# Optimization experiments

Hardware: AMD Instinct MI355X
Metric: run time of the kernel (lower is better)

Reference implementation:

```python
import jax, jax.numpy as jnp
import numpy as np
from jax import lax

POOL_SIZES = (1, 3, 5, 7, 14)  # PyramidSample bins -> 1+9+25+49+196 = 280 positions


def _pool_mat(in_size, out_size):
    # exact torch adaptive_avg_pool1d bin boundaries as a [out, in] averaging matrix
    P = np.zeros((out_size, in_size), np.float32)
    for i in range(out_size):
        s = (i * in_size) // out_size
        e = -((-(i + 1) * in_size) // out_size)
        P[i, s:e] = 1.0 / (e - s)
    return jnp.asarray(P)


def _psp(x):
    # x: [B, C, H, W] -> [B, C, 280]
    B, C, H, W = x.shape
    outs = []
    for s in POOL_SIZES:
        Ph, Pw = _pool_mat(H, s), _pool_mat(W, s)
        y = jnp.einsum('oh,bchw,pw->bcop', Ph, x, Pw)  # adaptive avg pool to [s,s]
        outs.append(y.reshape(B, C, s * s))
    return jnp.concatenate(outs, axis=-1)


def setup_inputs() -> dict:
    key = jax.random.key(0)
    ks = jax.random.split(key, 7)
    B, C, H, W = 8, 256, 96, 96
    c8 = max(4, C // 8)  # 32
    return {
        'x_1': jax.random.normal(ks[0], (B, C, H, W), jnp.float32),
        'x':   jax.random.normal(ks[1], (B, C, H, W), jnp.float32),
        'wq':  jax.random.normal(ks[2], (C, C), jnp.float32) * 0.05,
        'bq':  jax.random.normal(ks[3], (C,), jnp.float32) * 0.05,
        'wk':  jax.random.normal(ks[4], (c8, C), jnp.float32) * 0.05,
        'bk':  jax.random.normal(ks[5], (c8,), jnp.float32) * 0.05,
        'con': jax.random.normal(ks[6], (c8, C, 3, 3), jnp.float32),
    }


def reference(x_1, x, wq, bq, wk, bk, con):
    B, C, H, W = x.shape
    c8 = wk.shape[0]
    # 1x1 convs
    q = jnp.einsum('oc,bchw->bohw', wq, x_1) + bq[None, :, None, None]
    k = jnp.einsum('oc,bchw->bohw', wk, x) + bk[None, :, None, None]
    proj_query = _psp(q)                         # [B, C, 280]
    proj_key = _psp(k)                           # [B, c8, 280]
    aff = jax.nn.sigmoid(jnp.einsum('bcp,bkp->bck', proj_query, proj_key))  # [B, C, c8]
    # synthesize per-sample dynamic 3x3 weights: [B*C, C, 3, 3]
    agg_w = (aff.reshape(B * C, c8) @ con.reshape(c8, C * 9)).reshape(B * C, C, 3, 3)
    # grouped conv, groups = B
    xg = x_1.reshape(1, B * C, H, W)
    out = lax.conv_general_dilated(
        xg, agg_w, window_strides=(1, 1), padding=((1, 1), (1, 1)),
        dimension_numbers=('NCHW', 'OIHW', 'NCHW'), feature_group_count=B)
    return out.reshape(B, C, H, W)
```

## Files before the change

### kernel.cpp

```cpp
#include <hip/hip_runtime.h>
#include <hip/hip_bf16.h>


#define B 8
#define C 256
#define C8 32
#define H 96
#define W 96
#define HW 9216
#define NPOS 280
#define NP 288
#define NWBIN 30
#define RPS 108
#define OTS 68
#define XCH 260
#define PJS 304

typedef __attribute__((ext_vector_type(8))) short short8;
typedef __attribute__((ext_vector_type(4))) float float4v;
typedef __attribute__((ext_vector_type(4))) unsigned short ushort4v;

static __device__ __forceinline__ unsigned short f2bf(float f) {
    unsigned u = __float_as_uint(f);
    unsigned r = (u + 0x7FFF + ((u >> 16) & 1)) >> 16;
    return (unsigned short)r;
}
static __device__ __forceinline__ float bf2f(unsigned short h) {
    unsigned u = ((unsigned)h) << 16;
    return __uint_as_float(u);
}

template<int H0>
static __device__ __forceinline__ void accum_half_col(const float* __restrict__ col0,
                                                      float acc[NWBIN]) {
    const int SC[5]   = {1, 3, 5, 7, 14};
    const int WOFF[5] = {0, 1, 4, 9, 16};
    #pragma unroll
    for (int k = 0; k < NWBIN; ++k) acc[k] = 0.f;
    #pragma unroll
    for (int g = 0; g < 4; ++g) {
        float v[12];
        #pragma unroll
        for (int q = 0; q < 12; ++q) v[q] = col0[(size_t)(H0 + g * 12 + q) * 96];
        #pragma unroll
        for (int q = 0; q < 12; ++q) {
            const int h = H0 + g * 12 + q;
            #pragma unroll
            for (int si = 0; si < 5; ++si) {
                #pragma unroll
                for (int j = 0; j < SC[si]; ++j) {
                    const int st = (j * 96) / SC[si];
                    const int en = (96 * (j + 1) + SC[si] - 1) / SC[si];
                    if (h >= st && h < en) acc[WOFF[si] + j] += v[q];
                }
            }
        }
    }
}

__global__ __launch_bounds__(256) void pool_kernel(const float* __restrict__ x1,
                                                   const float* __restrict__ x,
                                                   unsigned short* __restrict__ px1t,
                                                   unsigned short* __restrict__ pxt) {
    __shared__ __align__(16) float colp[NWBIN * RPS];
    const int bi = blockIdx.x;
    const int which = bi >> 11;
    const int bc = bi & 2047;
    const float* __restrict__ src = (which ? x : x1) + (size_t)bc * HW;
    const int b = bc >> 8;
    const int c = bc & 255;
    unsigned short* __restrict__ dstT = (which ? pxt : px1t) + ((size_t)b * NP) * C + c;
    const int tid = threadIdx.x;

    const int SC[5]   = {1, 3, 5, 7, 14};
    const int WOFF[5] = {0, 1, 4, 9, 16};
    const int POFF[5] = {0, 1, 10, 35, 84};

    float acc[NWBIN];
    if (tid < 96) {
        accum_half_col<0>(src + tid, acc);
    } else if (tid >= 128 && tid < 224) {
        accum_half_col<48>(src + (tid - 128), acc);
    }

    if (tid >= 128 && tid < 224) {
        const int w1 = tid - 128;
        #pragma unroll
        for (int si = 0; si < 5; ++si) {
            #pragma unroll
            for (int i = 0; i < SC[si]; ++i)
                colp[(WOFF[si] + i) * RPS + w1] = acc[WOFF[si] + i];
        }
    }
    __syncthreads();
    if (tid < 96) {
        #pragma unroll
        for (int si = 0; si < 5; ++si) {
            #pragma unroll
            for (int i = 0; i < SC[si]; ++i) {
                const int st = (i * 96) / SC[si];
                const int en = (96 * (i + 1) + SC[si] - 1) / SC[si];
                const float inv = 1.0f / (float)(en - st);
                const int bin = WOFF[si] + i;
                colp[bin * RPS + tid] = (acc[bin] + colp[bin * RPS + tid]) * inv;
            }
        }
    }
    __syncthreads();

    if (tid < NWBIN) {
        float run = 0.f;
        #pragma unroll
        for (int cc = 0; cc < 24; ++cc) {
            float4 v = *(const float4*)&colp[tid * RPS + 4 * cc];
            v.x += run; v.y += v.x; v.z += v.y; v.w += v.z;
            run = v.w;
            *(float4*)&colp[tid * RPS + 4 * cc] = v;
        }
    }
    __syncthreads();

    for (int p = tid; p < NPOS; p += 256) {
        int si;
        if (p < 1) si = 0; else if (p < 10) si = 1; else if (p < 35) si = 2;
        else if (p < 84) si = 3; else si = 4;
        int s = SC[si];
        int loc = p - POFF[si];
        int i = loc / s;
        int j = loc - i * s;
        int st = (j * 96) / s;
        int en = (96 * (j + 1) + s - 1) / s;
        int binrow = WOFF[si] + i;
        float hi = colp[binrow * RPS + (en - 1)];
        float lo = (st > 0) ? colp[binrow * RPS + (st - 1)] : 0.f;
        dstT[(size_t)p * C] = f2bf((hi - lo) * (1.0f / (float)(en - st)));
    }
    if (tid < NP - NPOS) dstT[(size_t)(NPOS + tid) * C] = 0;
}

__global__ __launch_bounds__(256) void proj_mfma(const unsigned short* __restrict__ px1t,
                                                 const unsigned short* __restrict__ pxt,
                                                 const float* __restrict__ wq,
                                                 const float* __restrict__ bq,
                                                 const float* __restrict__ wk,
                                                 const float* __restrict__ bk,
                                                 unsigned short* __restrict__ PQb,
                                                 unsigned short* __restrict__ PKb) {
    __shared__ __align__(16) unsigned short lds[16 * PJS];
    const int bi = blockIdx.x;
    const int b = bi / 18;
    const int mt = bi % 18;
    const int tid = threadIdx.x;
    const int wid = tid >> 6;
    const int lane = tid & 63;
    const int n = lane & 15, quad = lane >> 4;
    const bool isQ = (mt < 16);
    const int row0 = isQ ? mt * 16 : (mt - 16) * 16;
    const float* __restrict__ wm = isQ ? wq : wk;
    const float* __restrict__ bias = isQ ? bq : bk;
    const unsigned short* __restrict__ src = (isQ ? px1t : pxt) + (size_t)b * NP * C;

    short8 af[8];
    #pragma unroll
    for (int ks = 0; ks < 8; ++ks) {
        const float* wr = &wm[(row0 + n) * C + ks * 32 + quad * 8];
        short8 a;
        #pragma unroll
        for (int j = 0; j < 8; ++j) a[j] = (short)f2bf(wr[j]);
        af[ks] = a;
    }

    float4v acc[5];
    #pragma unroll
    for (int t = 0; t < 5; ++t) acc[t] = (float4v){0.f, 0.f, 0.f, 0.f};

    #pragma unroll
    for (int t = 0; t < 5; ++t) {
        const int nt = t * 4 + wid;
        if (nt < 18) {
            #pragma unroll
            for (int ks = 0; ks < 8; ++ks) {
                short8 bf = *(const short8*)&src[(size_t)(nt * 16 + n) * C + ks * 32 + quad * 8];
                acc[t] = __builtin_amdgcn_mfma_f32_16x16x32_bf16(af[ks], bf, acc[t], 0, 0, 0);
            }
        }
    }

    #pragma unroll
    for (int t = 0; t < 5; ++t) {
        const int nt = t * 4 + wid;
        if (nt < 18) {
            #pragma unroll
            for (int reg = 0; reg < 4; ++reg) {
                float v = acc[t][reg] + bias[row0 + quad * 4 + reg];
                lds[(quad * 4 + reg) * PJS + nt * 16 + n] = f2bf(v);
            }
        }
    }
    __syncthreads();
    unsigned short* __restrict__ dstb = isQ ? PQb + ((size_t)b * C + row0) * NP
                                            : PKb + ((size_t)b * C8 + row0) * NP;
    for (int idx = tid; idx < 16 * 144; idx += 256) {
        int r = idx / 144;
        int c2 = idx - r * 144;
        unsigned int v = 0u;
        if (c2 < 140) v = *(const unsigned int*)&lds[r * PJS + c2 * 2];
        ((unsigned int*)&dstb[(size_t)r * NP])[c2] = v;
    }
}

__global__ __launch_bounds__(256) void aff_mfma(const unsigned short* __restrict__ PQb,
                                                const unsigned short* __restrict__ PKb,
                                                unsigned short* __restrict__ affb) {
    const int bi = blockIdx.x;
    const int b = bi >> 2;
    const int og = bi & 3;
    const int tid = threadIdx.x;
    const int wid = tid >> 6;
    const int lane = tid & 63;
    const int n = lane & 15, quad = lane >> 4;
    const int o = og * 64 + wid * 16 + n;

    float4v acc[2];
    acc[0] = (float4v){0.f, 0.f, 0.f, 0.f};
    acc[1] = (float4v){0.f, 0.f, 0.f, 0.f};

    #pragma unroll
    for (int ks = 0; ks < 9; ++ks) {
        short8 bfr = *(const short8*)&PQb[((size_t)b * C + o) * NP + ks * 32 + quad * 8];
        #pragma unroll
        for (int mt = 0; mt < 2; ++mt) {
            short8 a = *(const short8*)&PKb[((size_t)b * C8 + mt * 16 + n) * NP + ks * 32 + quad * 8];
            acc[mt] = __builtin_amdgcn_mfma_f32_16x16x32_bf16(a, bfr, acc[mt], 0, 0, 0);
        }
    }

    #pragma unroll
    for (int mt = 0; mt < 2; ++mt) {
        ushort4v v;
        #pragma unroll
        for (int reg = 0; reg < 4; ++reg) {
            float s = 1.0f / (1.0f + __expf(-acc[mt][reg]));
            v[reg] = f2bf(s);
        }
        *(ushort4v*)&affb[((size_t)b * C + o) * C8 + mt * 16 + quad * 4] = v;
    }
}

__global__ __launch_bounds__(256) void aswz_kernel(const float* __restrict__ con,
                                                   unsigned short* __restrict__ aswz) {
    int idx = blockIdx.x * 256 + threadIdx.x;
    if (idx >= 73728) return;
    int j = idx & 7;
    int lane = (idx >> 3) & 63;
    int mt = (idx >> 9) & 1;
    int s = idx >> 10;
    int pos = s >> 3;
    int cg = s & 7;
    int m = lane & 15, quad = lane >> 4;
    int ko = mt * 16 + m;
    int c = cg * 32 + quad * 8 + j;
    int dy = pos / 3, dx = pos - dy * 3;
    float v = con[((ko * C + c) * 3 + dy) * 3 + dx];
    aswz[idx] = f2bf(v);
}

__global__ __launch_bounds__(256) void x2bf_kernel(const float* __restrict__ x1,
                                                   unsigned short* __restrict__ xbf) {
    __shared__ __align__(16) unsigned short tl[64 * XCH];
    const int bi = blockIdx.x;
    const int b = bi / 144;
    const int pt = bi % 144;
    const int p0 = pt * 64;
    const int wid = threadIdx.x >> 6;
    const int lane = threadIdx.x & 63;

    #pragma unroll 8
    for (int it = 0; it < 64; ++it) {
        int ch = it * 4 + wid;
        float v = x1[((size_t)(b * C + ch)) * HW + p0 + lane];
        tl[lane * XCH + ch] = f2bf(v);
    }
    __syncthreads();
    #pragma unroll
    for (int it = 0; it < 16; ++it) {
        int pr = it * 4 + wid;
        ushort4v v = *(const ushort4v*)&tl[pr * XCH + lane * 4];
        *(ushort4v*)&xbf[((size_t)b * HW + p0 + pr) * 256 + lane * 4] = v;
    }
}

__global__ __launch_bounds__(256) void yconv_mfma(const unsigned short* __restrict__ xbf,
                                                  const unsigned short* __restrict__ aswz,
                                                  unsigned short* __restrict__ Yp) {
    __shared__ unsigned short xsl[10 * 50 * 40];
    const int bi = blockIdx.x;
    const int kc = bi & 3;
    const int rest = bi >> 2;
    const int tilex = rest & 1;
    const int tiley = (rest >> 1) % 12;
    const int b = rest / 24;
    const int tid = threadIdx.x;
    const int wid = tid >> 6;
    const int lane = tid & 63;
    const int n = lane & 15, quad = lane >> 4;

    float4v acc[2][6];
    #pragma unroll
    for (int mt = 0; mt < 2; ++mt)
        #pragma unroll
        for (int t = 0; t < 6; ++t)
            acc[mt][t] = (float4v){0.f, 0.f, 0.f, 0.f};

    int baseb[6];
    #pragma unroll
    for (int t = 0; t < 6; ++t) {
        int tt = wid * 6 + t;
        int rt = tt / 3;
        int xb = (tt % 3) * 16;
        baseb[t] = (rt * 50 + xb + n) * 40 + quad * 8;
    }

    for (int ci = 0; ci < 2; ++ci) {
        const int cg = kc * 2 + ci;
        __syncthreads();
        for (int task = tid; task < 2000; task += 256) {
            int pix = task >> 2;
            int cq = task & 3;
            int r = pix / 50;
            int col = pix - r * 50;
            int gy = tiley * 8 + r - 1;
            int gx = tilex * 48 + col - 1;
            uint4 v = make_uint4(0u, 0u, 0u, 0u);
            if ((unsigned)gy < 96u && (unsigned)gx < 96u)
                v = *(const uint4*)&xbf[((size_t)b * HW + gy * 96 + gx) * 256 + cg * 32 + cq * 8];
            *(uint4*)&xsl[(r * 50 + col) * 40 + cq * 8] = v;
        }
        short8 af[9][2];
        #pragma unroll
        for (int pos = 0; pos < 9; ++pos)
            #pragma unroll
            for (int mt = 0; mt < 2; ++mt)
                af[pos][mt] = *(const short8*)&aswz[((((pos * 8 + cg) * 2) + mt) * 64 + lane) * 8];
        __syncthreads();

        #pragma unroll
        for (int pos = 0; pos < 9; ++pos) {
            const int dy = pos / 3, dx = pos - (pos / 3) * 3;
            const int d = (dy * 50 + dx) * 40;
            #pragma unroll
            for (int t = 0; t < 6; ++t) {
                short8 bf = *(const short8*)&xsl[baseb[t] + d];
                acc[0][t] = __builtin_amdgcn_mfma_f32_16x16x32_bf16(af[pos][0], bf, acc[0][t], 0, 0, 0);
                acc[1][t] = __builtin_amdgcn_mfma_f32_16x16x32_bf16(af[pos][1], bf, acc[1][t], 0, 0, 0);
            }
        }
    }

    #pragma unroll
    for (int mt = 0; mt < 2; ++mt) {
        #pragma unroll
        for (int t = 0; t < 6; ++t) {
            int tt = wid * 6 + t;
            int rt = tt / 3;
            int xb = (tt % 3) * 16;
            int gy = tiley * 8 + rt;
            int gx = tilex * 48 + xb + n;
            ushort4v v;
            #pragma unroll
            for (int reg = 0; reg < 4; ++reg) v[reg] = f2bf(acc[mt][t][reg]);
            *(ushort4v*)&Yp[((((size_t)kc * B + b) * HW + gy * 96 + gx)) * C8 + mt * 16 + quad * 4] = v;
        }
    }
}

__global__ __launch_bounds__(256) void mix_kernel(const unsigned short* __restrict__ Yp,
                                                  const unsigned short* __restrict__ affb,
                                                  float* __restrict__ out) {
    __shared__ float ot[128 * OTS];
    const int bi = blockIdx.x;
    const int b = bi / 144;
    const int pg = bi % 144;
    const int wid = threadIdx.x >> 6;
    const int lane = threadIdx.x & 63;
    const int n = lane & 15, quad = lane >> 4;
    const int px0 = pg * 64 + wid * 16;

    short8 y0 = *(const short8*)&Yp[(((size_t)0 * B + b) * HW + px0 + n) * C8 + quad * 8];
    short8 y1 = *(const short8*)&Yp[(((size_t)1 * B + b) * HW + px0 + n) * C8 + quad * 8];
    short8 y2 = *(const short8*)&Yp[(((size_t)2 * B + b) * HW + px0 + n) * C8 + quad * 8];
    short8 y3 = *(const short8*)&Yp[(((size_t)3 * B + b) * HW + px0 + n) * C8 + quad * 8];

    float4v acc[16];
    #pragma unroll
    for (int mt = 0; mt < 16; ++mt) acc[mt] = (float4v){0.f, 0.f, 0.f, 0.f};

    #pragma unroll
    for (int mt = 0; mt < 16; ++mt) {
        const short8 a = *(const short8*)&affb[((size_t)b * C + mt * 16 + n) * C8 + quad * 8];
        acc[mt] = __builtin_amdgcn_mfma_f32_16x16x32_bf16(a, y0, acc[mt], 0, 0, 0);
        acc[mt] = __builtin_amdgcn_mfma_f32_16x16x32_bf16(a, y1, acc[mt], 0, 0, 0);
        acc[mt] = __builtin_amdgcn_mfma_f32_16x16x32_bf16(a, y2, acc[mt], 0, 0, 0);
        acc[mt] = __builtin_amdgcn_mfma_f32_16x16x32_bf16(a, y3, acc[mt], 0, 0, 0);
    }

    #pragma unroll
    for (int half = 0; half < 2; ++half) {
        __syncthreads();
        #pragma unroll
        for (int mt = 0; mt < 8; ++mt) {
            #pragma unroll
            for (int reg = 0; reg < 4; ++reg) {
                ot[(mt * 16 + quad * 4 + reg) * OTS + wid * 16 + n] = acc[half * 8 + mt][reg];
            }
        }
        __syncthreads();
        #pragma unroll
        for (int i = 0; i < 32; ++i) {
            int o = wid * 32 + i;
            out[((size_t)b * C + half * 128 + o) * HW + pg * 64 + lane] = ot[o * OTS + lane];
        }
    }
}

extern "C" void kernel_launch(void* const* d_in, const int* in_sizes, int n_in,
                              void* d_out, int out_size, void* d_ws, size_t ws_size,
                              hipStream_t stream) {
    const float* x1  = (const float*)d_in[0];
    const float* x   = (const float*)d_in[1];
    const float* wq  = (const float*)d_in[2];
    const float* bq  = (const float*)d_in[3];
    const float* wk  = (const float*)d_in[4];
    const float* bk  = (const float*)d_in[5];
    const float* con = (const float*)d_in[6];
    float* out = (float*)d_out;

    float* ws = (float*)d_ws;
    unsigned short* affb = (unsigned short*)ws;
    unsigned short* aswz = (unsigned short*)(ws + 65536);
    unsigned short* px1t = (unsigned short*)(ws + 102400);
    unsigned short* pxt  = (unsigned short*)(ws + 397312);
    unsigned short* PQb  = (unsigned short*)(ws + 692224);
    unsigned short* PKb  = (unsigned short*)(ws + 987136);
    unsigned short* xbf = (unsigned short*)(ws + 102400);
    unsigned short* Yp  = (unsigned short*)(ws + 9539584);

    aswz_kernel<<<288, 256, 0, stream>>>(con, aswz);
    pool_kernel<<<4096, 256, 0, stream>>>(x1, x, px1t, pxt);
    proj_mfma<<<B * 18, 256, 0, stream>>>(px1t, pxt, wq, bq, wk, bk, PQb, PKb);
    aff_mfma<<<B * 4, 256, 0, stream>>>(PQb, PKb, affb);
    x2bf_kernel<<<1152, 256, 0, stream>>>(x1, xbf);
    yconv_mfma<<<768, 256, 0, stream>>>(xbf, aswz, Yp);
    mix_kernel<<<1152, 256, 0, stream>>>(Yp, affb, out);
}
```

Before: 269.6 us.

## Fuse independent pre-processing and affinity/conv kernels into combined launches

Merges the pooling, bf16 transpose of x_1 and weight swizzle kernels into one launch dispatched by block index, and merges the affinity GEMM with the dynamic conv kernel. The workspace layout is changed so xbf no longer aliases the pooled buffers, which lets the transpose run concurrently with pooling. The aim is to remove launch gaps and serialization between independent stages. The cost is that every block of the fused kernel reserves the largest shared-memory footprint, which may lower occupancy for pool blocks.

```diff
diff --git a/kernel.cpp b/kernel.cpp
--- a/kernel.cpp
+++ b/kernel.cpp
@@ -25,10 +25,6 @@
     unsigned r = (u + 0x7FFF + ((u >> 16) & 1)) >> 16;
     return (unsigned short)r;
 }
-static __device__ __forceinline__ float bf2f(unsigned short h) {
-    unsigned u = ((unsigned)h) << 16;
-    return __uint_as_float(u);
-}
 
 template<int H0>
 static __device__ __forceinline__ void accum_half_col(const float* __restrict__ col0,
@@ -58,12 +54,11 @@
     }
 }
 
-__global__ __launch_bounds__(256) void pool_kernel(const float* __restrict__ x1,
-                                                   const float* __restrict__ x,
-                                                   unsigned short* __restrict__ px1t,
-                                                   unsigned short* __restrict__ pxt) {
-    __shared__ __align__(16) float colp[NWBIN * RPS];
-    const int bi = blockIdx.x;
+static __device__ __forceinline__ void pool_body(int bi, const float* __restrict__ x1,
+                                                 const float* __restrict__ x,
+                                                 unsigned short* __restrict__ px1t,
+                                                 unsigned short* __restrict__ pxt,
+                                                 float* colp) {
     const int which = bi >> 11;
     const int bc = bi & 2047;
     const float* __restrict__ src = (which ? x : x1) + (size_t)bc * HW;
@@ -136,6 +131,65 @@
         dstT[(size_t)p * C] = f2bf((hi - lo) * (1.0f / (float)(en - st)));
     }
     if (tid < NP - NPOS) dstT[(size_t)(NPOS + tid) * C] = 0;
+}
+
+static __device__ __forceinline__ void x2bf_body(int bi, const float* __restrict__ x1,
+                                                 unsigned short* __restrict__ xbf,
+                                                 unsigned short* tl) {
+    const int b = bi / 144;
+    const int pt = bi % 144;
+    const int p0 = pt * 64;
+    const int wid = threadIdx.x >> 6;
+    const int lane = threadIdx.x & 63;
+
+    #pragma unroll 8
+    for (int it = 0; it < 64; ++it) {
+        int ch = it * 4 + wid;
+        float v = x1[((size_t)(b * C + ch)) * HW + p0 + lane];
+        tl[lane * XCH + ch] = f2bf(v);
+    }
+    __syncthreads();
+    #pragma unroll
+    for (int it = 0; it < 16; ++it) {
+        int pr = it * 4 + wid;
+        ushort4v v = *(const ushort4v*)&tl[pr * XCH + lane * 4];
+        *(ushort4v*)&xbf[((size_t)b * HW + p0 + pr) * 256 + lane * 4] = v;
+    }
+}
+
+static __device__ __forceinline__ void aswz_body(int idx, const float* __restrict__ con,
+                                                 unsigned short* __restrict__ aswz) {
+    if (idx >= 73728) return;
+    int j = idx & 7;
+    int lane = (idx >> 3) & 63;
+    int mt = (idx >> 9) & 1;
+    int s = idx >> 10;
+    int pos = s >> 3;
+    int cg = s & 7;
+    int m = lane & 15, quad = lane >> 4;
+    int ko = mt * 16 + m;
+    int c = cg * 32 + quad * 8 + j;
+    int dy = pos / 3, dx = pos - dy * 3;
+    float v = con[((ko * C + c) * 3 + dy) * 3 + dx];
+    aswz[idx] = f2bf(v);
+}
+
+__global__ __launch_bounds__(256) void fusedA(const float* __restrict__ x1,
+                                              const float* __restrict__ x,
+                                              const float* __restrict__ con,
+                                              unsigned short* __restrict__ px1t,
+                                              unsigned short* __restrict__ pxt,
+                                              unsigned short* __restrict__ xbf,
+                                              unsigned short* __restrict__ aswz) {
+    __shared__ __align__(16) unsigned char smem[64 * XCH * 2];
+    const int bi = blockIdx.x;
+    if (bi < 4096) {
+        pool_body(bi, x1, x, px1t, pxt, (float*)smem);
+    } else if (bi < 5248) {
+        x2bf_body(bi - 4096, x1, xbf, (unsigned short*)smem);
+    } else {
+        aswz_body((bi - 5248) * 256 + threadIdx.x, con, aswz);
+    }
 }
 
 __global__ __launch_bounds__(256) void proj_mfma(const unsigned short* __restrict__ px1t,
@@ -209,10 +263,9 @@
     }
 }
 
-__global__ __launch_bounds__(256) void aff_mfma(const unsigned short* __restrict__ PQb,
+static __device__ __forceinline__ void aff_body(int bi, const unsigned short* __restrict__ PQb,
                                                 const unsigned short* __restrict__ PKb,
                                                 unsigned short* __restrict__ affb) {
-    const int bi = blockIdx.x;
     const int b = bi >> 2;
     const int og = bi & 3;
     const int tid = threadIdx.x;
@@ -247,54 +300,10 @@
     }
 }
 
-__global__ __launch_bounds__(256) void aswz_kernel(const float* __restrict__ con,
-                                                   unsigned short* __restrict__ aswz) {
-    int idx = blockIdx.x * 256 + threadIdx.x;
-    if (idx >= 73728) return;
-    int j = idx & 7;
-    int lane = (idx >> 3) & 63;
-    int mt = (idx >> 9) & 1;
-    int s = idx >> 10;
-    int pos = s >> 3;
-    int cg = s & 7;
-    int m = lane & 15, quad = lane >> 4;
-    int ko = mt * 16 + m;
-    int c = cg * 32 + quad * 8 + j;
-    int dy = pos / 3, dx = pos - dy * 3;
-    float v = con[((ko * C + c) * 3 + dy) * 3 + dx];
-    aswz[idx] = f2bf(v);
-}
-
-__global__ __launch_bounds__(256) void x2bf_kernel(const float* __restrict__ x1,
-                                                   unsigned short* __restrict__ xbf) {
-    __shared__ __align__(16) unsigned short tl[64 * XCH];
-    const int bi = blockIdx.x;
-    const int b = bi / 144;
-    const int pt = bi % 144;
-    const int p0 = pt * 64;
-    const int wid = threadIdx.x >> 6;
-    const int lane = threadIdx.x & 63;
-
-    #pragma unroll 8
-    for (int it = 0; it < 64; ++it) {
-        int ch = it * 4 + wid;
-        float v = x1[((size_t)(b * C + ch)) * HW + p0 + lane];
-        tl[lane * XCH + ch] = f2bf(v);
-    }
-    __syncthreads();
-    #pragma unroll
-    for (int it = 0; it < 16; ++it) {
-        int pr = it * 4 + wid;
-        ushort4v v = *(const ushort4v*)&tl[pr * XCH + lane * 4];
-        *(ushort4v*)&xbf[((size_t)b * HW + p0 + pr) * 256 + lane * 4] = v;
-    }
-}
-
-__global__ __launch_bounds__(256) void yconv_mfma(const unsigned short* __restrict__ xbf,
+static __device__ __forceinline__ void yconv_body(int bi, const unsigned short* __restrict__ xbf,
                                                   const unsigned short* __restrict__ aswz,
-                                                  unsigned short* __restrict__ Yp) {
-    __shared__ unsigned short xsl[10 * 50 * 40];
-    const int bi = blockIdx.x;
+                                                  unsigned short* __restrict__ Yp,
+                                                  unsigned short* xsl) {
     const int kc = bi & 3;
     const int rest = bi >> 2;
     const int tilex = rest & 1;
@@ -374,6 +383,21 @@
     }
 }
 
+__global__ __launch_bounds__(256) void fusedC(const unsigned short* __restrict__ PQb,
+                                              const unsigned short* __restrict__ PKb,
+                                              unsigned short* __restrict__ affb,
+                                              const unsigned short* __restrict__ xbf,
+                                              const unsigned short* __restrict__ aswz,
+                                              unsigned short* __restrict__ Yp) {
+    __shared__ __align__(16) unsigned short xsl[10 * 50 * 40];
+    const int bi = blockIdx.x;
+    if (bi < 32) {
+        aff_body(bi, PQb, PKb, affb);
+    } else {
+        yconv_body(bi - 32, xbf, aswz, Yp, xsl);
+    }
+}
+
 __global__ __launch_bounds__(256) void mix_kernel(const unsigned short* __restrict__ Yp,
                                                   const unsigned short* __restrict__ affb,
                                                   float* __restrict__ out) {
@@ -437,19 +461,16 @@
 
     float* ws = (float*)d_ws;
     unsigned short* affb = (unsigned short*)ws;
-    unsigned short* aswz = (unsigned short*)(ws + 65536);
-    unsigned short* px1t = (unsigned short*)(ws + 102400);
-    unsigned short* pxt  = (unsigned short*)(ws + 397312);
-    unsigned short* PQb  = (unsigned short*)(ws + 692224);
-    unsigned short* PKb  = (unsigned short*)(ws + 987136);
-    unsigned short* xbf = (unsigned short*)(ws + 102400);
-    unsigned short* Yp  = (unsigned short*)(ws + 9539584);
-
-    aswz_kernel<<<288, 256, 0, stream>>>(con, aswz);
-    pool_kernel<<<4096, 256, 0, stream>>>(x1, x, px1t, pxt);
+    unsigned short* aswz = (unsigned short*)(ws + 32768);
+    unsigned short* PQb  = (unsigned short*)(ws + 69632);
+    unsigned short* PKb  = (unsigned short*)(ws + 364544);
+    unsigned short* xbf  = (unsigned short*)(ws + 401408);
+    unsigned short* px1t = (unsigned short*)(ws + 9838592);
+    unsigned short* pxt  = (unsigned short*)(ws + 10133504);
+    unsigned short* Yp   = (unsigned short*)(ws + 9838592);
+
+    fusedA<<<5536, 256, 0, stream>>>(x1, x, con, px1t, pxt, xbf, aswz);
     proj_mfma<<<B * 18, 256, 0, stream>>>(px1t, pxt, wq, bq, wk, bk, PQb, PKb);
-    aff_mfma<<<B * 4, 256, 0, stream>>>(PQb, PKb, affb);
-    x2bf_kernel<<<1152, 256, 0, stream>>>(x1, xbf);
-    yconv_mfma<<<768, 256, 0, stream>>>(xbf, aswz, Yp);
+    fusedC<<<32 + 768, 256, 0, stream>>>(PQb, PKb, affb, xbf, aswz, Yp);
     mix_kernel<<<1152, 256, 0, stream>>>(Yp, affb, out);
 }
```

Result: faster. 259.1 us (-3.9%).
